# Optimization experiments

Measured on AMD Instinct MI355X. Metric: run time of the kernel, lower is better.

## Reference

```python
import jax, jax.numpy as jnp
import numpy as np
import math

BATCH = 4096
DIM_FEATURES = 4096
NEURONS_HL = 4096
NUM_LABELS = 1024

def _init_binary_linear(key, in_features, out_features):
    stdv = math.sqrt(1.5 / (in_features + out_features))
    w = jax.random.uniform(key, (out_features, in_features), jnp.float32, -stdv, stdv)
    b = jnp.zeros((out_features,), jnp.float32)
    return w, b

def setup_inputs() -> dict:
    key = jax.random.key(0)
    kx, k1, k2 = jax.random.split(key, 3)
    x = jax.random.normal(kx, (BATCH, DIM_FEATURES), jnp.float32)
    w1, b1 = _init_binary_linear(k1, DIM_FEATURES, NEURONS_HL)
    w2, b2 = _init_binary_linear(k2, NEURONS_HL, NUM_LABELS)
    return {"x": x, "w1": w1, "b1": b1, "w2": w2, "b2": b2}

def binarize(w):
    # sign binarization; map sign(0) -> +1 to match common Binarize impls
    return jnp.where(w >= 0, 1.0, -1.0).astype(w.dtype)

def reference(x, w1, b1, w2, b2):
    # fc1: binarized-weight linear + ReLU
    h = jax.nn.relu(jnp.einsum('bi,oi->bo', x, binarize(w1)) + b1)
    # fc2: binarized-weight linear
    out = jnp.einsum('bh,oh->bo', h, binarize(w2)) + b2
    return out
```

## Files before the change

kernel.cpp:

```cpp
#include <hip/hip_runtime.h>
#include <hip/hip_bf16.h>
#include <stdint.h>

typedef __bf16 bf16x8 __attribute__((ext_vector_type(8)));
typedef float  f32x4  __attribute__((ext_vector_type(4)));
typedef unsigned short ushortx8 __attribute__((ext_vector_type(8)));

#define LDS_B(p) ((__attribute__((address_space(3))) void*)(p))
#define GLB_B(p) ((const __attribute__((address_space(1))) void*)(p))

__device__ __forceinline__ unsigned short f2bf_rn(float f) {
  union { float f; uint32_t u; } v; v.f = f;
  uint32_t u = v.u;
  u += 0x7FFFu + ((u >> 16) & 1u);
  return (unsigned short)(u >> 16);
}


__global__ void cvt_f32_to_bf16(const float* __restrict__ in,
                                unsigned short* __restrict__ out, int n) {
  int i = (blockIdx.x * 256 + threadIdx.x) * 8;
  if (i >= n) return;
  const float4 f0 = *(const float4*)(in + i);
  const float4 f1 = *(const float4*)(in + i + 4);
  ushortx8 o;
  o[0] = f2bf_rn(f0.x); o[1] = f2bf_rn(f0.y);
  o[2] = f2bf_rn(f0.z); o[3] = f2bf_rn(f0.w);
  o[4] = f2bf_rn(f1.x); o[5] = f2bf_rn(f1.y);
  o[6] = f2bf_rn(f1.z); o[7] = f2bf_rn(f1.w);
  *(ushortx8*)(out + i) = o;
}

__global__ void binarize_to_bf16(const float* __restrict__ in,
                                 unsigned short* __restrict__ out, int n) {
  int i = (blockIdx.x * 256 + threadIdx.x) * 8;
  if (i >= n) return;
  const float4 f0 = *(const float4*)(in + i);
  const float4 f1 = *(const float4*)(in + i + 4);
  ushortx8 o;
  o[0] = f0.x >= 0.f ? 0x3F80 : 0xBF80;
  o[1] = f0.y >= 0.f ? 0x3F80 : 0xBF80;
  o[2] = f0.z >= 0.f ? 0x3F80 : 0xBF80;
  o[3] = f0.w >= 0.f ? 0x3F80 : 0xBF80;
  o[4] = f1.x >= 0.f ? 0x3F80 : 0xBF80;
  o[5] = f1.y >= 0.f ? 0x3F80 : 0xBF80;
  o[6] = f1.z >= 0.f ? 0x3F80 : 0xBF80;
  o[7] = f1.w >= 0.f ? 0x3F80 : 0xBF80;
  *(ushortx8*)(out + i) = o;
}


template <int MODE>
__global__ __launch_bounds__(256, 2)
void gemm_bt_128(const unsigned short* __restrict__ A,
                 const unsigned short* __restrict__ B,
                 const float* __restrict__ bias,
                 void* __restrict__ C,
                 int M, int N, int K, int KS)
{
  __shared__ unsigned short As[2][128][32];
  __shared__ unsigned short Bs[2][128][32];

  const int tid  = threadIdx.x;
  const int wid  = tid >> 6;
  const int lane = tid & 63;

  const int row0 = blockIdx.x * 128;
  const int col0 = blockIdx.y * 128;
  const int kOff = (MODE == 2) ? blockIdx.z * KS : 0;
  const int kLen = (MODE == 2) ? KS : K;

  const int srow = tid >> 2;
  const int scol = (tid & 3) << 3;

  const size_t aBase = (size_t)(row0 + srow) * K + scol + kOff;
  const size_t bBase = (size_t)(col0 + srow) * K + scol + kOff;
  const int ldsWaveOff = wid << 10;

  const int fr = lane & 15;
  const int fq = lane >> 4;
  const int wr = (wid >> 1) * 64;
  const int wc = (wid & 1) * 64;

  f32x4 acc[4][4] = {};

  const int nt = kLen >> 5;

  auto stage = [&](int buf, int t) {
    const size_t k0 = (size_t)t << 5;
    const unsigned short* a0 = A + aBase + k0;
    const unsigned short* a1 = a0 + (size_t)64 * K;
    const unsigned short* b0 = B + bBase + k0;
    const unsigned short* b1 = b0 + (size_t)64 * K;
    char* aL = (char*)&As[buf][0][0] + ldsWaveOff;
    char* bL = (char*)&Bs[buf][0][0] + ldsWaveOff;
    __builtin_amdgcn_global_load_lds(GLB_B(a0), LDS_B(aL),        16, 0, 0);
    __builtin_amdgcn_global_load_lds(GLB_B(a1), LDS_B(aL + 4096), 16, 0, 0);
    __builtin_amdgcn_global_load_lds(GLB_B(b0), LDS_B(bL),        16, 0, 0);
    __builtin_amdgcn_global_load_lds(GLB_B(b1), LDS_B(bL + 4096), 16, 0, 0);
  };

  auto compute = [&](int buf) {
    bf16x8 af[4], bq[4];
#pragma unroll
    for (int mi = 0; mi < 4; ++mi)
      af[mi] = *(const bf16x8*)&As[buf][wr + mi * 16 + fr][fq << 3];
#pragma unroll
    for (int ni = 0; ni < 4; ++ni)
      bq[ni] = *(const bf16x8*)&Bs[buf][wc + ni * 16 + fr][fq << 3];
#pragma unroll
    for (int mi = 0; mi < 4; ++mi)
#pragma unroll
      for (int ni = 0; ni < 4; ++ni)
        acc[mi][ni] = __builtin_amdgcn_mfma_f32_16x16x32_bf16(
            af[mi], bq[ni], acc[mi][ni], 0, 0, 0);
  };

  stage(0, 0);
  __syncthreads();

  int cur = 0;
  for (int t = 0; t < nt - 1; ++t) {
    stage(cur ^ 1, t + 1);
    compute(cur);
    __syncthreads();
    cur ^= 1;
  }
  compute(cur);

  float bv[4];
  if (MODE == 0) {
#pragma unroll
    for (int ni = 0; ni < 4; ++ni)
      bv[ni] = bias[col0 + wc + ni * 16 + fr];
  }

  float* Cz = (MODE == 2)
      ? ((float*)C + (size_t)blockIdx.z * M * N)
      : (float*)C;

#pragma unroll
  for (int mi = 0; mi < 4; ++mi) {
#pragma unroll
    for (int ni = 0; ni < 4; ++ni) {
      const int c = col0 + wc + ni * 16 + fr;
#pragma unroll
      for (int j = 0; j < 4; ++j) {
        const int r = row0 + wr + mi * 16 + fq * 4 + j;
        if (MODE == 0) {
          float v = acc[mi][ni][j] + bv[ni];
          v = v > 0.f ? v : 0.f;
          ((unsigned short*)C)[(size_t)r * N + c] = f2bf_rn(v);
        } else {
          Cz[(size_t)r * N + c] = acc[mi][ni][j];
        }
      }
    }
  }
}


__global__ void reduce4_bias(const float4* __restrict__ P,
                             const float* __restrict__ bias,
                             float4* __restrict__ out,
                             int MN4, int n4mask) {
  int j = blockIdx.x * 256 + threadIdx.x;
  if (j >= MN4) return;
  float4 a = P[j];
  float4 b = P[j + MN4];
  float4 c = P[j + 2 * MN4];
  float4 d = P[j + 3 * MN4];
  float4 bv = *(const float4*)(bias + ((j & n4mask) << 2));
  float4 o;
  o.x = (a.x + b.x) + (c.x + d.x) + bv.x;
  o.y = (a.y + b.y) + (c.y + d.y) + bv.y;
  o.z = (a.z + b.z) + (c.z + d.z) + bv.z;
  o.w = (a.w + b.w) + (c.w + d.w) + bv.w;
  out[j] = o;
}


extern "C" void kernel_launch(void* const* d_in, const int* in_sizes, int n_in,
                              void* d_out, int out_size, void* d_ws, size_t ws_size,
                              hipStream_t stream) {
  const float* x  = (const float*)d_in[0];
  const float* w1 = (const float*)d_in[1];
  const float* b1 = (const float*)d_in[2];
  const float* w2 = (const float*)d_in[3];
  const float* b2 = (const float*)d_in[4];
  float* out = (float*)d_out;

  constexpr int M = 4096, K = 4096, H = 4096, O = 1024;
  constexpr int SPLITS = 4;

  char* ws = (char*)d_ws;
  unsigned short* xb   = (unsigned short*)(ws);
  unsigned short* w1b  = (unsigned short*)(ws + (size_t)33554432);
  unsigned short* w2b  = (unsigned short*)(ws + (size_t)67108864);
  unsigned short* hb   = (unsigned short*)(ws + (size_t)75497472);
  float*          part = (float*)(ws);

  cvt_f32_to_bf16 <<<(M * K / 8 + 255) / 256, 256, 0, stream>>>(x,  xb,  M * K);
  binarize_to_bf16<<<(H * K / 8 + 255) / 256, 256, 0, stream>>>(w1, w1b, H * K);
  binarize_to_bf16<<<(O * H / 8 + 255) / 256, 256, 0, stream>>>(w2, w2b, O * H);

  gemm_bt_128<0><<<dim3(M / 128, H / 128), 256, 0, stream>>>(
      xb, w1b, b1, (void*)hb, M, H, K, 0);

  gemm_bt_128<2><<<dim3(M / 128, O / 128, SPLITS), 256, 0, stream>>>(
      hb, w2b, nullptr, (void*)part, M, O, H, H / SPLITS);

  constexpr int MN4 = M * O / 4;
  reduce4_bias<<<(MN4 + 255) / 256, 256, 0, stream>>>(
      (const float4*)part, b2, (float4*)out, MN4, O / 4 - 1);
}
```

Before: 365.1 us.

## Replace fc1 GEMM with 256x256-tile, 8-wave, phased-pipeline kernel with swizzled LDS

```diff
diff --git a/kernel.cpp b/kernel.cpp
--- a/kernel.cpp
+++ b/kernel.cpp
@@ -50,13 +50,168 @@
 }
 
 
-template <int MODE>
-__global__ __launch_bounds__(256, 2)
-void gemm_bt_128(const unsigned short* __restrict__ A,
+#define BAR()   asm volatile("s_barrier" ::: "memory")
+#define LGKM0() asm volatile("s_waitcnt lgkmcnt(0)" ::: "memory")
+#define VM4()   asm volatile("s_waitcnt vmcnt(4)" ::: "memory")
+#define VM0()   asm volatile("s_waitcnt vmcnt(0)" ::: "memory")
+
+__global__ __launch_bounds__(512, 2)
+void gemm256_8ph(const unsigned short* __restrict__ A,
                  const unsigned short* __restrict__ B,
                  const float* __restrict__ bias,
-                 void* __restrict__ C,
-                 int M, int N, int K, int KS)
+                 unsigned short* __restrict__ C,
+                 int M, int N, int K)
+{
+  __shared__ char lds[131072];
+
+  const int tid  = threadIdx.x;
+  const int wid  = tid >> 6;
+  const int lane = tid & 63;
+  const int wm   = wid >> 2;
+  const int wn   = wid & 3;
+
+  const int nbn  = N >> 8;
+  const int cpx  = gridDim.x >> 3;
+  const int bid  = blockIdx.x;
+  const int swzb = (bid & 7) * cpx + (bid >> 3);
+  const int row0 = (swzb / nbn) << 8;
+  const int col0 = (swzb % nbn) << 8;
+
+  const int fr = lane & 15;
+  const int fq = lane >> 4;
+
+  const int sRow  = lane >> 3;
+  const int sColE = ((lane & 7) ^ sRow) << 3;
+
+  char* const L = lds;
+
+  auto stageA = [&](int buf, int h, int t) {
+#pragma unroll
+    for (int r = 0; r < 2; ++r) {
+      const unsigned short* src =
+          A + (size_t)(row0 + h * 128 + r * 64 + wid * 8 + sRow) * K + t * 64 + sColE;
+      __builtin_amdgcn_global_load_lds(GLB_B(src),
+          LDS_B(L + buf * 65536 + h * 16384 + r * 8192 + wid * 1024), 16, 0, 0);
+    }
+  };
+  auto stageB = [&](int buf, int h, int t) {
+#pragma unroll
+    for (int r = 0; r < 2; ++r) {
+      const unsigned short* src =
+          B + (size_t)(col0 + h * 128 + r * 64 + wid * 8 + sRow) * K + t * 64 + sColE;
+      __builtin_amdgcn_global_load_lds(GLB_B(src),
+          LDS_B(L + buf * 65536 + 32768 + h * 16384 + r * 8192 + wid * 1024), 16, 0, 0);
+    }
+  };
+
+  const int keyx = (fr & 7) << 4;
+  auto ldA = [&](int buf, int mf, int ks) -> bf16x8 {
+    return *(const bf16x8*)(L + buf * 65536 + wm * 16384
+        + (mf * 16 + fr) * 128 + (((ks * 64) + (fq << 4)) ^ keyx));
+  };
+  auto ldB = [&](int buf, int nf, int ks) -> bf16x8 {
+    return *(const bf16x8*)(L + buf * 65536 + 32768 + (wn >> 1) * 16384
+        + ((wn & 1) * 64 + nf * 16 + fr) * 128 + (((ks * 64) + (fq << 4)) ^ keyx));
+  };
+
+  f32x4  acc[8][4] = {};
+  bf16x8 aF[4][2], bF[4][2];
+
+  const int NT = K >> 6;
+
+  stageA(0, 0, 0); stageA(0, 1, 0);
+  stageB(0, 0, 0); stageB(0, 1, 0);
+  stageB(1, 0, 1); stageB(1, 1, 1);
+  VM4(); BAR();
+
+  for (int t = 0; t < NT; ++t) {
+    const int buf = t & 1;
+#pragma unroll
+    for (int mi = 0; mi < 4; ++mi) { aF[mi][0] = ldA(buf, mi, 0); aF[mi][1] = ldA(buf, mi, 1); }
+#pragma unroll
+    for (int ni = 0; ni < 2; ++ni) { bF[ni][0] = ldB(buf, ni, 0); bF[ni][1] = ldB(buf, ni, 1); }
+    if (t + 1 < NT) stageA(buf ^ 1, 0, t + 1);
+    BAR(); LGKM0();
+    __builtin_amdgcn_s_setprio(1);
+#pragma unroll
+    for (int mi = 0; mi < 4; ++mi)
+#pragma unroll
+      for (int ni = 0; ni < 2; ++ni) {
+        acc[mi][ni] = __builtin_amdgcn_mfma_f32_16x16x32_bf16(aF[mi][0], bF[ni][0], acc[mi][ni], 0, 0, 0);
+        acc[mi][ni] = __builtin_amdgcn_mfma_f32_16x16x32_bf16(aF[mi][1], bF[ni][1], acc[mi][ni], 0, 0, 0);
+      }
+    __builtin_amdgcn_s_setprio(0);
+    BAR();
+#pragma unroll
+    for (int ni = 2; ni < 4; ++ni) { bF[ni][0] = ldB(buf, ni, 0); bF[ni][1] = ldB(buf, ni, 1); }
+    if (t + 1 < NT) stageA(buf ^ 1, 1, t + 1);
+    BAR(); LGKM0();
+    __builtin_amdgcn_s_setprio(1);
+#pragma unroll
+    for (int mi = 0; mi < 4; ++mi)
+#pragma unroll
+      for (int ni = 2; ni < 4; ++ni) {
+        acc[mi][ni] = __builtin_amdgcn_mfma_f32_16x16x32_bf16(aF[mi][0], bF[ni][0], acc[mi][ni], 0, 0, 0);
+        acc[mi][ni] = __builtin_amdgcn_mfma_f32_16x16x32_bf16(aF[mi][1], bF[ni][1], acc[mi][ni], 0, 0, 0);
+      }
+    __builtin_amdgcn_s_setprio(0);
+    BAR();
+#pragma unroll
+    for (int mi = 0; mi < 4; ++mi) { aF[mi][0] = ldA(buf, mi + 4, 0); aF[mi][1] = ldA(buf, mi + 4, 1); }
+    if (t + 2 < NT) stageB(buf, 0, t + 2);
+    BAR(); LGKM0();
+    __builtin_amdgcn_s_setprio(1);
+#pragma unroll
+    for (int mi = 0; mi < 4; ++mi)
+#pragma unroll
+      for (int ni = 2; ni < 4; ++ni) {
+        acc[mi + 4][ni] = __builtin_amdgcn_mfma_f32_16x16x32_bf16(aF[mi][0], bF[ni][0], acc[mi + 4][ni], 0, 0, 0);
+        acc[mi + 4][ni] = __builtin_amdgcn_mfma_f32_16x16x32_bf16(aF[mi][1], bF[ni][1], acc[mi + 4][ni], 0, 0, 0);
+      }
+    __builtin_amdgcn_s_setprio(0);
+    BAR();
+    if (t + 2 < NT) stageB(buf, 1, t + 2);
+    BAR();
+    __builtin_amdgcn_s_setprio(1);
+#pragma unroll
+    for (int mi = 0; mi < 4; ++mi)
+#pragma unroll
+      for (int ni = 0; ni < 2; ++ni) {
+        acc[mi + 4][ni] = __builtin_amdgcn_mfma_f32_16x16x32_bf16(aF[mi][0], bF[ni][0], acc[mi + 4][ni], 0, 0, 0);
+        acc[mi + 4][ni] = __builtin_amdgcn_mfma_f32_16x16x32_bf16(aF[mi][1], bF[ni][1], acc[mi + 4][ni], 0, 0, 0);
+      }
+    __builtin_amdgcn_s_setprio(0);
+    if (t < NT - 2) { VM4(); } else { VM0(); }
+    BAR();
+  }
+
+  float bv[4];
+#pragma unroll
+  for (int ni = 0; ni < 4; ++ni)
+    bv[ni] = bias[col0 + wn * 64 + ni * 16 + fr];
+
+#pragma unroll
+  for (int mi = 0; mi < 8; ++mi) {
+#pragma unroll
+    for (int ni = 0; ni < 4; ++ni) {
+      const int c = col0 + wn * 64 + ni * 16 + fr;
+#pragma unroll
+      for (int j = 0; j < 4; ++j) {
+        const int r = row0 + wm * 128 + mi * 16 + fq * 4 + j;
+        float v = acc[mi][ni][j] + bv[ni];
+        v = v > 0.f ? v : 0.f;
+        C[(size_t)r * N + c] = f2bf_rn(v);
+      }
+    }
+  }
+}
+
+
+__global__ __launch_bounds__(256, 2)
+void gemm_bt_128_splitk(const unsigned short* __restrict__ A,
+                        const unsigned short* __restrict__ B,
+                        float* __restrict__ P,
+                        int M, int N, int K, int KS)
 {
   __shared__ unsigned short As[2][128][32];
   __shared__ unsigned short Bs[2][128][32];
@@ -67,8 +222,7 @@
 
   const int row0 = blockIdx.x * 128;
   const int col0 = blockIdx.y * 128;
-  const int kOff = (MODE == 2) ? blockIdx.z * KS : 0;
-  const int kLen = (MODE == 2) ? KS : K;
+  const int kOff = blockIdx.z * KS;
 
   const int srow = tid >> 2;
   const int scol = (tid & 3) << 3;
@@ -83,8 +237,7 @@
   const int wc = (wid & 1) * 64;
 
   f32x4 acc[4][4] = {};
-
-  const int nt = kLen >> 5;
+  const int nt = KS >> 5;
 
   auto stage = [&](int buf, int t) {
     const size_t k0 = (size_t)t << 5;
@@ -128,35 +281,18 @@
   }
   compute(cur);
 
-  float bv[4];
-  if (MODE == 0) {
-#pragma unroll
-    for (int ni = 0; ni < 4; ++ni)
-      bv[ni] = bias[col0 + wc + ni * 16 + fr];
-  }
-
-  float* Cz = (MODE == 2)
-      ? ((float*)C + (size_t)blockIdx.z * M * N)
-      : (float*)C;
-
-#pragma unroll
-  for (int mi = 0; mi < 4; ++mi) {
+  float* Pz = P + (size_t)blockIdx.z * M * N;
+#pragma unroll
+  for (int mi = 0; mi < 4; ++mi)
 #pragma unroll
     for (int ni = 0; ni < 4; ++ni) {
       const int c = col0 + wc + ni * 16 + fr;
 #pragma unroll
       for (int j = 0; j < 4; ++j) {
         const int r = row0 + wr + mi * 16 + fq * 4 + j;
-        if (MODE == 0) {
-          float v = acc[mi][ni][j] + bv[ni];
-          v = v > 0.f ? v : 0.f;
-          ((unsigned short*)C)[(size_t)r * N + c] = f2bf_rn(v);
-        } else {
-          Cz[(size_t)r * N + c] = acc[mi][ni][j];
-        }
+        Pz[(size_t)r * N + c] = acc[mi][ni][j];
       }
     }
-  }
 }
 
 
@@ -204,11 +340,10 @@
   binarize_to_bf16<<<(H * K / 8 + 255) / 256, 256, 0, stream>>>(w1, w1b, H * K);
   binarize_to_bf16<<<(O * H / 8 + 255) / 256, 256, 0, stream>>>(w2, w2b, O * H);
 
-  gemm_bt_128<0><<<dim3(M / 128, H / 128), 256, 0, stream>>>(
-      xb, w1b, b1, (void*)hb, M, H, K, 0);
-
-  gemm_bt_128<2><<<dim3(M / 128, O / 128, SPLITS), 256, 0, stream>>>(
-      hb, w2b, nullptr, (void*)part, M, O, H, H / SPLITS);
+  gemm256_8ph<<<(M / 256) * (H / 256), 512, 0, stream>>>(xb, w1b, b1, hb, M, H, K);
+
+  gemm_bt_128_splitk<<<dim3(M / 128, O / 128, SPLITS), 256, 0, stream>>>(
+      hb, w2b, part, M, O, H, H / SPLITS);
 
   constexpr int MN4 = M * O / 4;
   reduce4_bias<<<(MN4 + 255) / 256, 256, 0, stream>>>(
```

New measurement: 344.9 us. -5.5%, faster.

## Replace 128x128 GEMM with 256x256 eight-wave pipelined tile kernel

Applied to the files above, without the earlier changes.

```diff
diff --git a/kernel.cpp b/kernel.cpp
--- a/kernel.cpp
+++ b/kernel.cpp
@@ -50,112 +50,170 @@
 }
 
 
+#define BAR()  asm volatile("s_barrier" ::: "memory")
+#define VM4()  asm volatile("s_waitcnt vmcnt(4)" ::: "memory")
+#define VM2()  asm volatile("s_waitcnt vmcnt(2)" ::: "memory")
+#define VM0()  asm volatile("s_waitcnt vmcnt(0)" ::: "memory")
+#define PRIO1  __builtin_amdgcn_s_setprio(1)
+#define PRIO0  __builtin_amdgcn_s_setprio(0)
+
 template <int MODE>
-__global__ __launch_bounds__(256, 2)
-void gemm_bt_128(const unsigned short* __restrict__ A,
+__global__ __launch_bounds__(512, 2)
+void gemm256_8ph(const unsigned short* __restrict__ A,
                  const unsigned short* __restrict__ B,
                  const float* __restrict__ bias,
-                 void* __restrict__ C,
+                 void* __restrict__ Cv,
                  int M, int N, int K, int KS)
 {
-  __shared__ unsigned short As[2][128][32];
-  __shared__ unsigned short Bs[2][128][32];
+  __shared__ char lds[131072];
 
   const int tid  = threadIdx.x;
   const int wid  = tid >> 6;
   const int lane = tid & 63;
-
-  const int row0 = blockIdx.x * 128;
-  const int col0 = blockIdx.y * 128;
-  const int kOff = (MODE == 2) ? blockIdx.z * KS : 0;
-  const int kLen = (MODE == 2) ? KS : K;
-
-  const int srow = tid >> 2;
-  const int scol = (tid & 3) << 3;
-
-  const size_t aBase = (size_t)(row0 + srow) * K + scol + kOff;
-  const size_t bBase = (size_t)(col0 + srow) * K + scol + kOff;
-  const int ldsWaveOff = wid << 10;
+  const int wm   = wid >> 2;
+  const int wn   = wid & 3;
+
+  const int nbn  = N >> 8;
+  const int cpx  = gridDim.x >> 3;
+  const int bid  = blockIdx.x;
+  const int swzb = (bid & 7) * cpx + (bid >> 3);
+  const int row0 = (swzb / nbn) << 8;
+  const int col0 = (swzb % nbn) << 8;
+  const int kOff = (MODE == 1) ? blockIdx.y * KS : 0;
 
   const int fr = lane & 15;
   const int fq = lane >> 4;
-  const int wr = (wid >> 1) * 64;
-  const int wc = (wid & 1) * 64;
-
-  f32x4 acc[4][4] = {};
-
-  const int nt = kLen >> 5;
-
-  auto stage = [&](int buf, int t) {
-    const size_t k0 = (size_t)t << 5;
-    const unsigned short* a0 = A + aBase + k0;
-    const unsigned short* a1 = a0 + (size_t)64 * K;
-    const unsigned short* b0 = B + bBase + k0;
-    const unsigned short* b1 = b0 + (size_t)64 * K;
-    char* aL = (char*)&As[buf][0][0] + ldsWaveOff;
-    char* bL = (char*)&Bs[buf][0][0] + ldsWaveOff;
-    __builtin_amdgcn_global_load_lds(GLB_B(a0), LDS_B(aL),        16, 0, 0);
-    __builtin_amdgcn_global_load_lds(GLB_B(a1), LDS_B(aL + 4096), 16, 0, 0);
-    __builtin_amdgcn_global_load_lds(GLB_B(b0), LDS_B(bL),        16, 0, 0);
-    __builtin_amdgcn_global_load_lds(GLB_B(b1), LDS_B(bL + 4096), 16, 0, 0);
-  };
-
-  auto compute = [&](int buf) {
-    bf16x8 af[4], bq[4];
+
+  const int sRow  = lane >> 3;
+  const int sColE = ((lane & 7) ^ sRow) << 3;
+
+  char* const L = lds;
+
+  auto stageA = [&](int buf, int h, int t) {
+#pragma unroll
+    for (int r = 0; r < 2; ++r) {
+      const unsigned short* src =
+          A + (size_t)(row0 + h * 128 + r * 64 + wid * 8 + sRow) * K + kOff + t * 64 + sColE;
+      __builtin_amdgcn_global_load_lds(GLB_B(src),
+          LDS_B(L + buf * 65536 + h * 16384 + r * 8192 + wid * 1024), 16, 0, 0);
+    }
+  };
+  auto stageB = [&](int buf, int h, int t) {
+#pragma unroll
+    for (int r = 0; r < 2; ++r) {
+      const unsigned short* src =
+          B + (size_t)(col0 + h * 128 + r * 64 + wid * 8 + sRow) * K + kOff + t * 64 + sColE;
+      __builtin_amdgcn_global_load_lds(GLB_B(src),
+          LDS_B(L + buf * 65536 + 32768 + h * 16384 + r * 8192 + wid * 1024), 16, 0, 0);
+    }
+  };
+
+  const int keyx = (fr & 7) << 4;
+  auto ldA = [&](int buf, int mf, int ks) -> bf16x8 {
+    return *(const bf16x8*)(L + buf * 65536 + wm * 16384
+        + (mf * 16 + fr) * 128 + (((ks * 64) + (fq << 4)) ^ keyx));
+  };
+  auto ldB = [&](int buf, int nf, int ks) -> bf16x8 {
+    return *(const bf16x8*)(L + buf * 65536 + 32768 + (wn >> 1) * 16384
+        + ((wn & 1) * 64 + nf * 16 + fr) * 128 + (((ks * 64) + (fq << 4)) ^ keyx));
+  };
+
+  f32x4  acc[8][4] = {};
+  bf16x8 aF[4][2], bF[4][2];
+
+  const int NT = KS >> 6;
+
+  auto quad = [&](int mbase, int n0) {
 #pragma unroll
     for (int mi = 0; mi < 4; ++mi)
-      af[mi] = *(const bf16x8*)&As[buf][wr + mi * 16 + fr][fq << 3];
+#pragma unroll
+      for (int d = 0; d < 2; ++d) {
+        const int ni = n0 + d;
+        acc[mbase + mi][ni] = __builtin_amdgcn_mfma_f32_16x16x32_bf16(
+            aF[mi][0], bF[ni][0], acc[mbase + mi][ni], 0, 0, 0);
+        acc[mbase + mi][ni] = __builtin_amdgcn_mfma_f32_16x16x32_bf16(
+            aF[mi][1], bF[ni][1], acc[mbase + mi][ni], 0, 0, 0);
+      }
+  };
+
+  auto tile = [&](int b, int t) {
+    aF[0][0] = ldA(b, 0, 0); bF[0][0] = ldB(b, 0, 0);
+    aF[1][0] = ldA(b, 1, 0); bF[1][0] = ldB(b, 1, 0);
+    aF[2][0] = ldA(b, 2, 0); aF[3][0] = ldA(b, 3, 0);
+    aF[0][1] = ldA(b, 0, 1); bF[0][1] = ldB(b, 0, 1);
+    aF[1][1] = ldA(b, 1, 1); bF[1][1] = ldB(b, 1, 1);
+    aF[2][1] = ldA(b, 2, 1); aF[3][1] = ldA(b, 3, 1);
+    if (t + 1 < NT) stageA(b ^ 1, 0, t + 1);
+    BAR();
+    PRIO1; quad(0, 0); PRIO0;
+    BAR();
+    if (t + 1 < NT) stageA(b ^ 1, 1, t + 1);
+    BAR();
+    PRIO1; quad(0, 2); PRIO0;
+    BAR();
+    aF[0][0] = ldA(b, 4, 0); aF[1][0] = ldA(b, 5, 0);
+    aF[2][0] = ldA(b, 6, 0); aF[3][0] = ldA(b, 7, 0);
+    aF[0][1] = ldA(b, 4, 1); aF[1][1] = ldA(b, 5, 1);
+    aF[2][1] = ldA(b, 6, 1); aF[3][1] = ldA(b, 7, 1);
+    if (t + 2 < NT) stageB(b, 0, t + 2);
+    BAR();
+    PRIO1; quad(4, 2); PRIO0;
+    if (t < NT - 2) { VM2(); } else { VM0(); }
+    BAR();
+    if (t + 1 < NT) {
+      bF[2][0] = ldB(b ^ 1, 2, 0); bF[3][0] = ldB(b ^ 1, 3, 0);
+      bF[2][1] = ldB(b ^ 1, 2, 1); bF[3][1] = ldB(b ^ 1, 3, 1);
+    }
+    if (t + 2 < NT) stageB(b, 1, t + 2);
+    BAR();
+    PRIO1; quad(4, 0); PRIO0;
+    BAR();
+  };
+
+  stageA(0, 0, 0); stageA(0, 1, 0);
+  stageB(0, 0, 0); stageB(0, 1, 0);
+  stageB(1, 0, 1); stageB(1, 1, 1);
+  VM4(); BAR();
+  bF[2][0] = ldB(0, 2, 0); bF[3][0] = ldB(0, 3, 0);
+  bF[2][1] = ldB(0, 2, 1); bF[3][1] = ldB(0, 3, 1);
+
+  for (int it = 0; it < (NT >> 1); ++it) {
+    tile(0, 2 * it);
+    tile(1, 2 * it + 1);
+  }
+
+  if (MODE == 0) {
+    unsigned short* C = (unsigned short*)Cv;
+    float bv[4];
 #pragma unroll
     for (int ni = 0; ni < 4; ++ni)
-      bq[ni] = *(const bf16x8*)&Bs[buf][wc + ni * 16 + fr][fq << 3];
-#pragma unroll
-    for (int mi = 0; mi < 4; ++mi)
-#pragma unroll
-      for (int ni = 0; ni < 4; ++ni)
-        acc[mi][ni] = __builtin_amdgcn_mfma_f32_16x16x32_bf16(
-            af[mi], bq[ni], acc[mi][ni], 0, 0, 0);
-  };
-
-  stage(0, 0);
-  __syncthreads();
-
-  int cur = 0;
-  for (int t = 0; t < nt - 1; ++t) {
-    stage(cur ^ 1, t + 1);
-    compute(cur);
-    __syncthreads();
-    cur ^= 1;
-  }
-  compute(cur);
-
-  float bv[4];
-  if (MODE == 0) {
-#pragma unroll
-    for (int ni = 0; ni < 4; ++ni)
-      bv[ni] = bias[col0 + wc + ni * 16 + fr];
-  }
-
-  float* Cz = (MODE == 2)
-      ? ((float*)C + (size_t)blockIdx.z * M * N)
-      : (float*)C;
-
-#pragma unroll
-  for (int mi = 0; mi < 4; ++mi) {
-#pragma unroll
-    for (int ni = 0; ni < 4; ++ni) {
-      const int c = col0 + wc + ni * 16 + fr;
-#pragma unroll
-      for (int j = 0; j < 4; ++j) {
-        const int r = row0 + wr + mi * 16 + fq * 4 + j;
-        if (MODE == 0) {
+      bv[ni] = bias[col0 + wn * 64 + ni * 16 + fr];
+#pragma unroll
+    for (int mi = 0; mi < 8; ++mi)
+#pragma unroll
+      for (int ni = 0; ni < 4; ++ni) {
+        const int c = col0 + wn * 64 + ni * 16 + fr;
+#pragma unroll
+        for (int j = 0; j < 4; ++j) {
+          const int r = row0 + wm * 128 + mi * 16 + fq * 4 + j;
           float v = acc[mi][ni][j] + bv[ni];
           v = v > 0.f ? v : 0.f;
-          ((unsigned short*)C)[(size_t)r * N + c] = f2bf_rn(v);
-        } else {
-          Cz[(size_t)r * N + c] = acc[mi][ni][j];
+          C[(size_t)r * N + c] = f2bf_rn(v);
         }
       }
-    }
+  } else {
+    float* P = (float*)Cv + (size_t)blockIdx.y * M * N;
+#pragma unroll
+    for (int mi = 0; mi < 8; ++mi)
+#pragma unroll
+      for (int ni = 0; ni < 4; ++ni) {
+        const int c = col0 + wn * 64 + ni * 16 + fr;
+#pragma unroll
+        for (int j = 0; j < 4; ++j) {
+          const int r = row0 + wm * 128 + mi * 16 + fq * 4 + j;
+          P[(size_t)r * N + c] = acc[mi][ni][j];
+        }
+      }
   }
 }
 
@@ -204,10 +262,10 @@
   binarize_to_bf16<<<(H * K / 8 + 255) / 256, 256, 0, stream>>>(w1, w1b, H * K);
   binarize_to_bf16<<<(O * H / 8 + 255) / 256, 256, 0, stream>>>(w2, w2b, O * H);
 
-  gemm_bt_128<0><<<dim3(M / 128, H / 128), 256, 0, stream>>>(
-      xb, w1b, b1, (void*)hb, M, H, K, 0);
-
-  gemm_bt_128<2><<<dim3(M / 128, O / 128, SPLITS), 256, 0, stream>>>(
+  gemm256_8ph<0><<<(M / 256) * (H / 256), 512, 0, stream>>>(
+      xb, w1b, b1, (void*)hb, M, H, K, K);
+
+  gemm256_8ph<1><<<dim3((M / 256) * (O / 256), SPLITS), 512, 0, stream>>>(
       hb, w2b, nullptr, (void*)part, M, O, H, H / SPLITS);
 
   constexpr int MN4 = M * O / 4;
```

New measurement: 333.7 us. -8.6%, faster.
